# Performance work log

Measured on AMD Instinct MI355X. Metric: run time of the kernel, lower is better.

The kernel has to match this reference:

```python
import jax, jax.numpy as jnp
import numpy as np

B, S, D = 2, 2048, 768
H = 12
DK = D // H  # 64; dim_q = dim_k = dim_v
DFF = 3072
EPS = 1e-5


def layer_norm(x, w, b):
    mu = jnp.mean(x, axis=-1, keepdims=True)
    var = jnp.var(x, axis=-1, keepdims=True)
    return (x - mu) * jax.lax.rsqrt(var + EPS) * w + b


def setup_inputs() -> dict:
    key = jax.random.key(0)
    ks = jax.random.split(key, 12)
    s = 0.02
    return {
        "src": jax.random.normal(ks[0], (B, S, D), dtype=jnp.float32),
        # per-head projections stacked over heads: [H, D, DK]
        "Wq": jax.random.normal(ks[1], (H, D, DK), dtype=jnp.float32) * s,
        "bq": jnp.zeros((H, DK), dtype=jnp.float32),
        "Wk": jax.random.normal(ks[2], (H, D, DK), dtype=jnp.float32) * s,
        "bk": jnp.zeros((H, DK), dtype=jnp.float32),
        "Wv": jax.random.normal(ks[3], (H, D, DK), dtype=jnp.float32) * s,
        "bv": jnp.zeros((H, DK), dtype=jnp.float32),
        # output projection: [H*DK, D]
        "Wo": jax.random.normal(ks[4], (H * DK, D), dtype=jnp.float32) * s,
        "bo": jnp.zeros((D,), dtype=jnp.float32),
        "ln1_w": jnp.ones((D,), dtype=jnp.float32),
        "ln1_b": jnp.zeros((D,), dtype=jnp.float32),
        "W1": jax.random.normal(ks[5], (D, DFF), dtype=jnp.float32) * s,
        "b1": jnp.zeros((DFF,), dtype=jnp.float32),
        "W2": jax.random.normal(ks[6], (DFF, D), dtype=jnp.float32) * s,
        "b2": jnp.zeros((D,), dtype=jnp.float32),
        "ln2_w": jnp.ones((D,), dtype=jnp.float32),
        "ln2_b": jnp.zeros((D,), dtype=jnp.float32),
    }


def reference(src, Wq, bq, Wk, bk, Wv, bv, Wo, bo, ln1_w, ln1_b,
              W1, b1, W2, b2, ln2_w, ln2_b):
    # per-head q/k/v projections, batched over heads via einsum
    q = jnp.einsum('bsd,hdk->bhsk', src, Wq) + bq[None, :, None, :]
    k = jnp.einsum('bsd,hdk->bhsk', src, Wk) + bk[None, :, None, :]
    v = jnp.einsum('bsd,hdk->bhsk', src, Wv) + bv[None, :, None, :]
    scale = jnp.asarray(DK, src.dtype) ** 0.5
    scores = jnp.einsum('bhsk,bhtk->bhst', q, k) / scale  # [B,H,S,S]
    attn = jax.nn.softmax(scores, axis=-1)
    ctx = jnp.einsum('bhst,bhtk->bhsk', attn, v)
    # concat heads along feature dim (matches torch.cat over head outputs)
    ctx = ctx.transpose(0, 2, 1, 3).reshape(src.shape[0], src.shape[1], H * DK)
    attn_out = ctx @ Wo + bo
    x = layer_norm(src + attn_out, ln1_w, ln1_b)
    ff = jax.nn.relu(x @ W1 + b1) @ W2 + b2
    return layer_norm(x + ff, ln2_w, ln2_b)
```

## Files before the change

kernel.cpp:

```cpp
#include <hip/hip_runtime.h>
#include <hip/hip_bf16.h>

#define S_LEN 2048
#define DMODEL 768
#define NHEAD 12
#define DKH 64
#define DFF_K 3072
#define MROWS 4096
#define KSPLIT 2
#define KHALF (S_LEN / KSPLIT)

typedef __attribute__((ext_vector_type(8))) short bf16x8;
typedef __attribute__((ext_vector_type(8))) unsigned short us8;
typedef __attribute__((ext_vector_type(4))) float f32x4;

__device__ __forceinline__ float bfu2f(unsigned short u) {
  return __uint_as_float(((unsigned int)u) << 16);
}
__device__ __forceinline__ unsigned short f2bfu(float f) {
  __hip_bfloat16 h = __float2bfloat16(f);
  return *reinterpret_cast<unsigned short*>(&h);
}

__global__ __launch_bounds__(256) void convert_kernel(
    const float* __restrict__ in, unsigned short* __restrict__ out, int n4)
{
  const int i = blockIdx.x * 256 + threadIdx.x;
  if (i < n4) {
    float4 v = *(const float4*)(in + (size_t)i * 4);
    ushort4 o;
    o.x = f2bfu(v.x); o.y = f2bfu(v.y); o.z = f2bfu(v.z); o.w = f2bfu(v.w);
    *(ushort4*)(out + (size_t)i * 4) = o;
  }
}

__device__ __forceinline__ void transpose_conv_body(
    const float* in, unsigned short* out, int R, int Ctot, int head,
    int bx, int by, int tid)
{
  __shared__ float t[64][68];
  const int r0 = bx * 64;
  const int c0 = by * 64;
  const float* ib;
  int ld;
  if (head) { ib = in + (size_t)by * R * 64; ld = 64; }
  else      { ib = in + c0;                  ld = Ctot; }
  const int lr = tid >> 4;
  const int lc = (tid & 15) << 2;

#pragma unroll
  for (int rr = 0; rr < 4; ++rr) {
    const int row = rr * 16 + lr;
    float4 v = *(const float4*)(ib + (size_t)(r0 + row) * ld + lc);
    t[row][lc + 0] = v.x; t[row][lc + 1] = v.y;
    t[row][lc + 2] = v.z; t[row][lc + 3] = v.w;
  }
  __syncthreads();
#pragma unroll
  for (int rr = 0; rr < 4; ++rr) {
    const int oc = rr * 16 + lr;
    ushort4 o;
    o.x = f2bfu(t[lc + 0][oc]); o.y = f2bfu(t[lc + 1][oc]);
    o.z = f2bfu(t[lc + 2][oc]); o.w = f2bfu(t[lc + 3][oc]);
    *(ushort4*)(out + (size_t)(c0 + oc) * R + r0 + lc) = o;
  }
}

__global__ __launch_bounds__(256) void transpose_conv_kernel(
    const float* __restrict__ in, unsigned short* __restrict__ out,
    int R, int Ctot, int head)
{
  transpose_conv_body(in, out, R, Ctot, head, blockIdx.x, blockIdx.y, threadIdx.x);
}

__global__ __launch_bounds__(256) void transpose_conv4_kernel(
    const float* __restrict__ i0, const float* __restrict__ i1,
    const float* __restrict__ i2, const float* __restrict__ i3,
    unsigned short* __restrict__ o0, unsigned short* __restrict__ o1,
    unsigned short* __restrict__ o2, unsigned short* __restrict__ o3)
{
  const int z = blockIdx.z;
  const float* in = (z == 0) ? i0 : (z == 1) ? i1 : (z == 2) ? i2 : i3;
  unsigned short* out = (z == 0) ? o0 : (z == 1) ? o1 : (z == 2) ? o2 : o3;
  transpose_conv_body(in, out, DMODEL, DMODEL, (z < 3) ? 1 : 0,
                      blockIdx.x, blockIdx.y, threadIdx.x);
}

template<int BN>
__global__ __launch_bounds__(256) void mfma_gemm_kernel(
    const unsigned short* __restrict__ A,
    const unsigned short* __restrict__ BT,
    const float* __restrict__ bias,
    unsigned short* __restrict__ C,
    int K, int N, int relu, int klen, size_t out_stride)
{
  constexpr int WN = (BN == 128) ? 64 : 32;
  constexpr int NJ = WN / 16;
  __shared__ unsigned short As[128][40];
  __shared__ unsigned short Bs[BN][40];

  const int tid  = threadIdx.x;
  const int wid  = tid >> 6;
  const int lane = tid & 63;
  const int ml   = lane & 15;
  const int quad = lane >> 4;
  const int wm   = (wid & 1) * 64;
  const int wn   = (wid >> 1) * WN;
  const int row0 = blockIdx.x * 128;
  const int col0 = blockIdx.y * BN;
  const int zed  = blockIdx.z;
  const int kb0  = zed * klen;
  const int kend = kb0 + klen;

  const int sr = tid >> 2;
  const int sk = (tid & 3) << 3;

  const unsigned short* pA0 = A  + (size_t)(row0 + sr) * K + sk;
  const unsigned short* pA1 = A  + (size_t)(row0 + sr + 64) * K + sk;
  const unsigned short* pB0 = BT + (size_t)(col0 + sr) * K + sk;
  const unsigned short* pB1 = BT + (size_t)(col0 + sr + 64) * K + sk;

  f32x4 acc[4][NJ];
#pragma unroll
  for (int i = 0; i < 4; ++i)
#pragma unroll
    for (int j = 0; j < NJ; ++j)
#pragma unroll
      for (int r = 0; r < 4; ++r) acc[i][j][r] = 0.f;

  us8 ra0 = *(const us8*)(pA0 + kb0);
  us8 ra1 = *(const us8*)(pA1 + kb0);
  us8 rb0 = *(const us8*)(pB0 + kb0);
  us8 rb1;
  if (BN == 128) rb1 = *(const us8*)(pB1 + kb0);

  for (int k0 = kb0; k0 < kend; k0 += 32) {
    *(us8*)&As[sr][sk]      = ra0;
    *(us8*)&As[sr + 64][sk] = ra1;
    *(us8*)&Bs[sr][sk]      = rb0;
    if (BN == 128) *(us8*)&Bs[sr + 64][sk] = rb1;
    __syncthreads();

    const int kn = k0 + 32;
    if (kn < kend) {
      ra0 = *(const us8*)(pA0 + kn);
      ra1 = *(const us8*)(pA1 + kn);
      rb0 = *(const us8*)(pB0 + kn);
      if (BN == 128) rb1 = *(const us8*)(pB1 + kn);
    }

    bf16x8 af[4], bfr[NJ];
#pragma unroll
    for (int i = 0; i < 4; ++i)
      af[i] = *(const bf16x8*)&As[wm + i * 16 + ml][quad << 3];
#pragma unroll
    for (int j = 0; j < NJ; ++j)
      bfr[j] = *(const bf16x8*)&Bs[wn + j * 16 + ml][quad << 3];
#pragma unroll
    for (int i = 0; i < 4; ++i)
#pragma unroll
      for (int j = 0; j < NJ; ++j)
        acc[i][j] = __builtin_amdgcn_mfma_f32_16x16x32_bf16(
            af[i], bfr[j], acc[i][j], 0, 0, 0);
    __syncthreads();
  }

  unsigned short* Cz = C + (size_t)zed * out_stride;
#pragma unroll
  for (int j = 0; j < NJ; ++j) {
    const int col = col0 + wn + j * 16 + ml;
    const float bb = (zed == 0) ? bias[col] : 0.f;
#pragma unroll
    for (int i = 0; i < 4; ++i) {
      const int r0g = row0 + wm + i * 16 + (quad << 2);
#pragma unroll
      for (int r = 0; r < 4; ++r) {
        float v = acc[i][j][r] + bb;
        if (relu) v = fmaxf(v, 0.f);
        Cz[(size_t)(r0g + r) * N + col] = f2bfu(v);
      }
    }
  }
}

__global__ __launch_bounds__(256) void qkv_gemm_kernel(
    const unsigned short* __restrict__ A,
    const unsigned short* __restrict__ W0, const unsigned short* __restrict__ W1,
    const unsigned short* __restrict__ W2,
    const float* __restrict__ bq, const float* __restrict__ bk,
    const float* __restrict__ bv,
    unsigned short* __restrict__ C0, unsigned short* __restrict__ C1,
    unsigned short* __restrict__ C2)
{
  __shared__ unsigned short As[128][40];
  __shared__ unsigned short Bs[64][40];
  const int z = blockIdx.z;
  const unsigned short* BT = (z == 0) ? W0 : (z == 1) ? W1 : W2;
  const float* bias = (z == 0) ? bq : (z == 1) ? bk : bv;
  unsigned short* C = (z == 0) ? C0 : (z == 1) ? C1 : C2;
  const int K = DMODEL, N = DMODEL;

  const int tid  = threadIdx.x;
  const int wid  = tid >> 6;
  const int lane = tid & 63;
  const int ml   = lane & 15;
  const int quad = lane >> 4;
  const int wm   = (wid & 1) * 64;
  const int wn   = (wid >> 1) * 32;
  const int row0 = blockIdx.x * 128;
  const int col0 = blockIdx.y * 64;
  const int sr = tid >> 2;
  const int sk = (tid & 3) << 3;

  const unsigned short* pA0 = A  + (size_t)(row0 + sr) * K + sk;
  const unsigned short* pA1 = A  + (size_t)(row0 + sr + 64) * K + sk;
  const unsigned short* pB0 = BT + (size_t)(col0 + sr) * K + sk;

  f32x4 acc[4][2];
#pragma unroll
  for (int i = 0; i < 4; ++i)
#pragma unroll
    for (int j = 0; j < 2; ++j)
#pragma unroll
      for (int r = 0; r < 4; ++r) acc[i][j][r] = 0.f;

  us8 ra0 = *(const us8*)pA0;
  us8 ra1 = *(const us8*)pA1;
  us8 rb0 = *(const us8*)pB0;

  for (int k0 = 0; k0 < K; k0 += 32) {
    *(us8*)&As[sr][sk]      = ra0;
    *(us8*)&As[sr + 64][sk] = ra1;
    *(us8*)&Bs[sr][sk]      = rb0;
    __syncthreads();

    const int kn = k0 + 32;
    if (kn < K) {
      ra0 = *(const us8*)(pA0 + kn);
      ra1 = *(const us8*)(pA1 + kn);
      rb0 = *(const us8*)(pB0 + kn);
    }

    bf16x8 af[4], bfr[2];
#pragma unroll
    for (int i = 0; i < 4; ++i)
      af[i] = *(const bf16x8*)&As[wm + i * 16 + ml][quad << 3];
#pragma unroll
    for (int j = 0; j < 2; ++j)
      bfr[j] = *(const bf16x8*)&Bs[wn + j * 16 + ml][quad << 3];
#pragma unroll
    for (int i = 0; i < 4; ++i)
#pragma unroll
      for (int j = 0; j < 2; ++j)
        acc[i][j] = __builtin_amdgcn_mfma_f32_16x16x32_bf16(
            af[i], bfr[j], acc[i][j], 0, 0, 0);
    __syncthreads();
  }

#pragma unroll
  for (int j = 0; j < 2; ++j) {
    const int col = col0 + wn + j * 16 + ml;
    const float bb = bias[col];
#pragma unroll
    for (int i = 0; i < 4; ++i) {
      const int r0g = row0 + wm + i * 16 + (quad << 2);
      if (z == 2) {
        const int bb_ = r0g >> 11, s = r0g & 2047;
        const int hh = col >> 6, dd = col & 63;
        ushort4 o;
        o.x = f2bfu(acc[i][j][0] + bb); o.y = f2bfu(acc[i][j][1] + bb);
        o.z = f2bfu(acc[i][j][2] + bb); o.w = f2bfu(acc[i][j][3] + bb);
        *(ushort4*)(C + ((size_t)((bb_ * NHEAD + hh) * DKH + dd)) * S_LEN + s) = o;
      } else {
#pragma unroll
        for (int r = 0; r < 4; ++r)
          C[(size_t)(r0g + r) * N + col] = f2bfu(acc[i][j][r] + bb);
      }
    }
  }
}

#define FATS 72
#define SCL2E 0.1803368822f
__global__ __launch_bounds__(256) void flash_attn_mfma(
    const unsigned short* __restrict__ Q,
    const unsigned short* __restrict__ K,
    const unsigned short* __restrict__ VT,
    float* __restrict__ Opart,
    float* __restrict__ Lpart)
{
  __shared__ unsigned short Ks[64][FATS];
  __shared__ unsigned short Vs[64][FATS];
  __shared__ unsigned short QP[4][16][FATS];

  const int tid  = threadIdx.x;
  const int wid  = tid >> 6;
  const int lane = tid & 63;
  const int ml   = lane & 15;
  const int quad = lane >> 4;
  const int h    = blockIdx.x, b = blockIdx.y;
  const int q0   = (blockIdx.z >> 1) * 64;
  const int ks   = blockIdx.z & 1;
  const int kt0  = ks * KHALF;

  const size_t qkbase = ((size_t)b * S_LEN) * DMODEL + (size_t)h * DKH;
  const size_t vtbase = ((size_t)(b * NHEAD + h)) * DKH * S_LEN;

  const int sr = tid >> 2;
  const int sc = (tid & 3) << 4;

  {
    const unsigned short* qp = Q + qkbase + (size_t)(q0 + sr) * DMODEL + sc;
    *(us8*)&QP[sr >> 4][sr & 15][sc]     = *(const us8*)qp;
    *(us8*)&QP[sr >> 4][sr & 15][sc + 8] = *(const us8*)(qp + 8);
  }
  bf16x8 qf[2];
  qf[0] = *(const bf16x8*)&QP[wid][ml][quad << 3];
  qf[1] = *(const bf16x8*)&QP[wid][ml][32 + (quad << 3)];

  const unsigned short* pK = K + qkbase + (size_t)(kt0 + sr) * DMODEL + sc;
  const unsigned short* pV = VT + vtbase + (size_t)sr * S_LEN + kt0 + sc;

  float lsum = 0.f;
  f32x4 oacc[4];
#pragma unroll
  for (int dt = 0; dt < 4; ++dt)
#pragma unroll
    for (int r = 0; r < 4; ++r) oacc[dt][r] = 0.f;

  us8 rk0 = *(const us8*)(pK);
  us8 rk1 = *(const us8*)(pK + 8);
  us8 rv0 = *(const us8*)(pV);
  us8 rv1 = *(const us8*)(pV + 8);

  for (int kt = 0; kt < KHALF; kt += 64) {
    __syncthreads();
    *(us8*)&Ks[sr][sc]     = rk0;
    *(us8*)&Ks[sr][sc + 8] = rk1;
    *(us8*)&Vs[sr][sc]     = rv0;
    *(us8*)&Vs[sr][sc + 8] = rv1;
    __syncthreads();

    const int ktn = kt + 64;
    if (ktn < KHALF) {
      rk0 = *(const us8*)(pK + (size_t)ktn * DMODEL);
      rk1 = *(const us8*)(pK + (size_t)ktn * DMODEL + 8);
      rv0 = *(const us8*)(pV + ktn);
      rv1 = *(const us8*)(pV + ktn + 8);
    }

    f32x4 sacc[4];
#pragma unroll
    for (int mt = 0; mt < 4; ++mt)
#pragma unroll
      for (int r = 0; r < 4; ++r) sacc[mt][r] = 0.f;
#pragma unroll
    for (int mt = 0; mt < 4; ++mt) {
      bf16x8 kf0 = *(const bf16x8*)&Ks[mt * 16 + ml][quad << 3];
      bf16x8 kf1 = *(const bf16x8*)&Ks[mt * 16 + ml][32 + (quad << 3)];
      sacc[mt] = __builtin_amdgcn_mfma_f32_16x16x32_bf16(kf0, qf[0], sacc[mt], 0, 0, 0);
      sacc[mt] = __builtin_amdgcn_mfma_f32_16x16x32_bf16(kf1, qf[1], sacc[mt], 0, 0, 0);
    }

    float p[4][4];
#pragma unroll
    for (int mt2 = 0; mt2 < 4; ++mt2)
#pragma unroll
      for (int r = 0; r < 4; ++r) {
        const float e = exp2f(sacc[mt2][r] * SCL2E);
        p[mt2][r] = e;
        lsum += e;
      }

#pragma unroll
    for (int mt2 = 0; mt2 < 4; ++mt2) {
      ushort4 o;
      o.x = f2bfu(p[mt2][0]); o.y = f2bfu(p[mt2][1]);
      o.z = f2bfu(p[mt2][2]); o.w = f2bfu(p[mt2][3]);
      *(ushort4*)&QP[wid][ml][mt2 * 16 + (quad << 2)] = o;
    }
    bf16x8 pf0 = *(const bf16x8*)&QP[wid][ml][quad << 3];
    bf16x8 pf1 = *(const bf16x8*)&QP[wid][ml][32 + (quad << 3)];

#pragma unroll
    for (int dt = 0; dt < 4; ++dt) {
      bf16x8 vf0 = *(const bf16x8*)&Vs[dt * 16 + ml][quad << 3];
      bf16x8 vf1 = *(const bf16x8*)&Vs[dt * 16 + ml][32 + (quad << 3)];
      oacc[dt] = __builtin_amdgcn_mfma_f32_16x16x32_bf16(vf0, pf0, oacc[dt], 0, 0, 0);
      oacc[dt] = __builtin_amdgcn_mfma_f32_16x16x32_bf16(vf1, pf1, oacc[dt], 0, 0, 0);
    }
  }

  lsum += __shfl_xor(lsum, 16);
  lsum += __shfl_xor(lsum, 32);
  const int qrow = q0 + wid * 16 + ml;
  const size_t obase =
      ((((size_t)(ks * 2 + b)) * NHEAD + h) * S_LEN + qrow) * DKH;
#pragma unroll
  for (int dt = 0; dt < 4; ++dt)
    *(f32x4*)&Opart[obase + dt * 16 + (quad << 2)] = oacc[dt];
  if (quad == 0)
    Lpart[(((size_t)(ks * 2 + b)) * NHEAD + h) * S_LEN + qrow] = lsum;
}

__global__ __launch_bounds__(256) void attn_combine_kernel(
    const float* __restrict__ Op,
    const float* __restrict__ Lp,
    unsigned short* __restrict__ O)
{
  const int s = blockIdx.x & (S_LEN - 1);
  const int b = blockIdx.x >> 11;
  const int tid = threadIdx.x;
  const size_t ohalf = (size_t)2 * NHEAD * S_LEN * DKH;
  const size_t lhalf = (size_t)2 * NHEAD * S_LEN;
#pragma unroll
  for (int c = tid; c < DMODEL; c += 256) {
    const int hh = c >> 6, dd = c & 63;
    const size_t li = ((size_t)b * NHEAD + hh) * S_LEN + s;
    const size_t oi = li * DKH + dd;
    const float o = Op[oi] + Op[ohalf + oi];
    const float l = Lp[li] + Lp[lhalf + li];
    O[((size_t)b * S_LEN + s) * DMODEL + c] = f2bfu(o / l);
  }
}

__global__ __launch_bounds__(256) void add_ln_kernel(
    const void* __restrict__ X, const void* __restrict__ Y,
    const void* __restrict__ Y2,
    const float* __restrict__ w, const float* __restrict__ bvec,
    void* __restrict__ out, int xbf, int ybf, int obf)
{
  __shared__ float buf[DMODEL];
  __shared__ float rbuf[8];
  const int tid  = threadIdx.x;
  const int lane = tid & 63, wv = tid >> 6;
  const size_t base = (size_t)blockIdx.x * DMODEL;

  float s = 0.f, s2 = 0.f;
#pragma unroll
  for (int j = tid; j < DMODEL; j += 256) {
    float xv = xbf ? bfu2f(((const unsigned short*)X)[base + j])
                   : ((const float*)X)[base + j];
    float yv = ybf ? bfu2f(((const unsigned short*)Y)[base + j])
                   : ((const float*)Y)[base + j];
    float v = xv + yv;
    if (Y2) v += ybf ? bfu2f(((const unsigned short*)Y2)[base + j])
                     : ((const float*)Y2)[base + j];
    buf[j] = v; s += v; s2 += v * v;
  }
#pragma unroll
  for (int o = 32; o; o >>= 1) { s += __shfl_xor(s, o); s2 += __shfl_xor(s2, o); }
  if (lane == 0) { rbuf[wv] = s; rbuf[4 + wv] = s2; }
  __syncthreads();
  const float S  = rbuf[0] + rbuf[1] + rbuf[2] + rbuf[3];
  const float S2 = rbuf[4] + rbuf[5] + rbuf[6] + rbuf[7];
  const float mean = S * (1.f / (float)DMODEL);
  const float var  = S2 * (1.f / (float)DMODEL) - mean * mean;
  const float rstd = rsqrtf(var + 1e-5f);
#pragma unroll
  for (int j = tid; j < DMODEL; j += 256) {
    float v = (buf[j] - mean) * rstd * w[j] + bvec[j];
    if (obf) ((unsigned short*)out)[base + j] = f2bfu(v);
    else     ((float*)out)[base + j] = v;
  }
}

extern "C" void kernel_launch(void* const* d_in, const int* in_sizes, int n_in,
                              void* d_out, int out_size, void* d_ws, size_t ws_size,
                              hipStream_t stream) {
  const float* src  = (const float*)d_in[0];
  const float* Wq   = (const float*)d_in[1];
  const float* bq   = (const float*)d_in[2];
  const float* Wk   = (const float*)d_in[3];
  const float* bk   = (const float*)d_in[4];
  const float* Wv   = (const float*)d_in[5];
  const float* bv   = (const float*)d_in[6];
  const float* Wo   = (const float*)d_in[7];
  const float* bo   = (const float*)d_in[8];
  const float* ln1w = (const float*)d_in[9];
  const float* ln1b = (const float*)d_in[10];
  const float* W1   = (const float*)d_in[11];
  const float* b1   = (const float*)d_in[12];
  const float* W2   = (const float*)d_in[13];
  const float* b2   = (const float*)d_in[14];
  const float* ln2w = (const float*)d_in[15];
  const float* ln2b = (const float*)d_in[16];
  (void)ws_size; (void)in_sizes; (void)n_in; (void)out_size;

  unsigned short* p = (unsigned short*)d_ws;
  const size_t SEG = (size_t)MROWS * DMODEL;
  unsigned short* srcb = p; p += SEG;
  unsigned short* qb   = p; p += SEG;
  unsigned short* kb_  = p; p += SEG;
  unsigned short* vbT  = p; p += SEG;
  unsigned short* ctx  = p; p += SEG;
  unsigned short* ff   = p; p += (size_t)MROWS * DFF_K;
  unsigned short* wqt  = p; p += (size_t)DMODEL * DMODEL;
  unsigned short* wkt  = p; p += (size_t)DMODEL * DMODEL;
  unsigned short* wvt  = p; p += (size_t)DMODEL * DMODEL;
  unsigned short* wot  = p; p += (size_t)DMODEL * DMODEL;
  unsigned short* w1t  = p; p += (size_t)DMODEL * DFF_K;
  unsigned short* w2t  = p; p += (size_t)DMODEL * DFF_K;
  unsigned short* x1 = kb_;
  float* opart = (float*)ff;
  float* lpart = (float*)wqt;

  dim3 blk(256);

  convert_kernel<<<dim3(SEG / 1024), blk, 0, stream>>>(src, srcb, (int)(SEG / 4));
  transpose_conv4_kernel<<<dim3(12, 12, 4), blk, 0, stream>>>(
      Wq, Wk, Wv, Wo, wqt, wkt, wvt, wot);
  transpose_conv_kernel<<<dim3(12, 48), blk, 0, stream>>>(W1, w1t, DMODEL, DFF_K, 0);
  transpose_conv_kernel<<<dim3(48, 12), blk, 0, stream>>>(W2, w2t, DFF_K, DMODEL, 0);

  dim3 gqkv(MROWS / 128, DMODEL / 64, 3);
  qkv_gemm_kernel<<<gqkv, blk, 0, stream>>>(srcb, wqt, wkt, wvt, bq, bk, bv,
                                            qb, kb_, vbT);

  dim3 ga(NHEAD, 2, (S_LEN / 64) * KSPLIT);
  flash_attn_mfma<<<ga, blk, 0, stream>>>(qb, kb_, vbT, opart, lpart);
  attn_combine_kernel<<<dim3(MROWS), blk, 0, stream>>>(opart, lpart, ctx);

  dim3 gWo(MROWS / 128, DMODEL / 64, 2);
  mfma_gemm_kernel<64><<<gWo, blk, 0, stream>>>(ctx, wot, bo, qb,
                                                DMODEL, DMODEL, 0, DMODEL / 2, 2 * SEG);

  add_ln_kernel<<<dim3(MROWS), blk, 0, stream>>>(srcb, qb, vbT,
                                                 ln1w, ln1b, x1, 1, 1, 1);

  dim3 gF1(MROWS / 128, DFF_K / 128, 1);
  mfma_gemm_kernel<128><<<gF1, blk, 0, stream>>>(x1, w1t, b1, ff,
                                                 DMODEL, DFF_K, 1, DMODEL, 0);

  dim3 gW2(MROWS / 128, DMODEL / 64, 2);
  mfma_gemm_kernel<64><<<gW2, blk, 0, stream>>>(ff, w2t, b2, qb,
                                                DFF_K, DMODEL, 0, DFF_K / 2, 2 * SEG);

  add_ln_kernel<<<dim3(MROWS), blk, 0, stream>>>(x1, qb, vbT,
                                                 ln2w, ln2b, (float*)d_out, 1, 1, 0);
}
```

Before: 305.9 us.

## Double query rows per flash-attention block and XOR-swizzle shared-memory tiles

Each wave now handles 32 query rows (two 16-row MFMA tiles) instead of 16, so every K/V tile staged in shared memory feeds twice as many MFMAs and the grid shrinks by half. The padded LDS arrays are replaced with unpadded 64-wide rows using an XOR swizzle to avoid bank conflicts. Q fragments are loaded straight from global memory into registers instead of going through LDS. Register pressure roughly doubles for accumulators, which the launch-bounds hint of 3 blocks per CU is meant to keep in check. The smaller grid also lowers parallelism.

```diff
diff --git a/kernel.cpp b/kernel.cpp
--- a/kernel.cpp
+++ b/kernel.cpp
@@ -280,18 +280,17 @@
   }
 }
 
-#define FATS 72
 #define SCL2E 0.1803368822f
-__global__ __launch_bounds__(256) void flash_attn_mfma(
+__global__ __launch_bounds__(256, 3) void flash_attn_mfma(
     const unsigned short* __restrict__ Q,
     const unsigned short* __restrict__ K,
     const unsigned short* __restrict__ VT,
     float* __restrict__ Opart,
     float* __restrict__ Lpart)
 {
-  __shared__ unsigned short Ks[64][FATS];
-  __shared__ unsigned short Vs[64][FATS];
-  __shared__ unsigned short QP[4][16][FATS];
+  __shared__ unsigned short Ks[64][64];
+  __shared__ unsigned short Vs[64][64];
+  __shared__ unsigned short QP[4][2][16][64];
 
   const int tid  = threadIdx.x;
   const int wid  = tid >> 6;
@@ -299,46 +298,53 @@
   const int ml   = lane & 15;
   const int quad = lane >> 4;
   const int h    = blockIdx.x, b = blockIdx.y;
-  const int q0   = (blockIdx.z >> 1) * 64;
+  const int q0   = (blockIdx.z >> 1) * 128;
   const int ks   = blockIdx.z & 1;
   const int kt0  = ks * KHALF;
 
   const size_t qkbase = ((size_t)b * S_LEN) * DMODEL + (size_t)h * DKH;
   const size_t vtbase = ((size_t)(b * NHEAD + h)) * DKH * S_LEN;
 
-  const int sr = tid >> 2;
-  const int sc = (tid & 3) << 4;
-
-  {
-    const unsigned short* qp = Q + qkbase + (size_t)(q0 + sr) * DMODEL + sc;
-    *(us8*)&QP[sr >> 4][sr & 15][sc]     = *(const us8*)qp;
-    *(us8*)&QP[sr >> 4][sr & 15][sc + 8] = *(const us8*)(qp + 8);
-  }
-  bf16x8 qf[2];
-  qf[0] = *(const bf16x8*)&QP[wid][ml][quad << 3];
-  qf[1] = *(const bf16x8*)&QP[wid][ml][32 + (quad << 3)];
-
-  const unsigned short* pK = K + qkbase + (size_t)(kt0 + sr) * DMODEL + sc;
-  const unsigned short* pV = VT + vtbase + (size_t)sr * S_LEN + kt0 + sc;
-
-  float lsum = 0.f;
-  f32x4 oacc[4];
+  const int sr  = tid >> 2;
+  const int scb = (tid & 3) << 5;
+  const int ssw = (sr & 7) << 4;
+  const int fsw = (ml & 7) << 4;
+
+  char* ksrow = (char*)&Ks[sr][0];
+  char* vsrow = (char*)&Vs[sr][0];
+
+  const int qrA = q0 + wid * 32 + ml;
+  const int qrB = qrA + 16;
+  const unsigned short* qpg = Q + qkbase;
+  bf16x8 qfA0 = *(const bf16x8*)(qpg + (size_t)qrA * DMODEL + (quad << 3));
+  bf16x8 qfA1 = *(const bf16x8*)(qpg + (size_t)qrA * DMODEL + 32 + (quad << 3));
+  bf16x8 qfB0 = *(const bf16x8*)(qpg + (size_t)qrB * DMODEL + (quad << 3));
+  bf16x8 qfB1 = *(const bf16x8*)(qpg + (size_t)qrB * DMODEL + 32 + (quad << 3));
+
+  const unsigned short* pK = K + qkbase + (size_t)(kt0 + sr) * DMODEL + (scb >> 1);
+  const unsigned short* pV = VT + vtbase + (size_t)sr * S_LEN + kt0 + (scb >> 1);
+
+  float lsumA = 0.f, lsumB = 0.f;
+  f32x4 oaccA[4], oaccB[4];
 #pragma unroll
   for (int dt = 0; dt < 4; ++dt)
 #pragma unroll
-    for (int r = 0; r < 4; ++r) oacc[dt][r] = 0.f;
+    for (int r = 0; r < 4; ++r) { oaccA[dt][r] = 0.f; oaccB[dt][r] = 0.f; }
 
   us8 rk0 = *(const us8*)(pK);
   us8 rk1 = *(const us8*)(pK + 8);
   us8 rv0 = *(const us8*)(pV);
   us8 rv1 = *(const us8*)(pV + 8);
 
+  char* qpA = (char*)&QP[wid][0][ml][0];
+  char* qpB = (char*)&QP[wid][1][ml][0];
+
   for (int kt = 0; kt < KHALF; kt += 64) {
     __syncthreads();
-    *(us8*)&Ks[sr][sc]     = rk0;
-    *(us8*)&Ks[sr][sc + 8] = rk1;
-    *(us8*)&Vs[sr][sc]     = rv0;
-    *(us8*)&Vs[sr][sc + 8] = rv1;
+    *(us8*)(ksrow + ((scb +  0) ^ ssw)) = rk0;
+    *(us8*)(ksrow + ((scb + 16) ^ ssw)) = rk1;
+    *(us8*)(vsrow + ((scb +  0) ^ ssw)) = rv0;
+    *(us8*)(vsrow + ((scb + 16) ^ ssw)) = rv1;
     __syncthreads();
 
     const int ktn = kt + 64;
@@ -349,58 +355,70 @@
       rv1 = *(const us8*)(pV + ktn + 8);
     }
 
-    f32x4 sacc[4];
+    f32x4 sA[4], sB[4];
 #pragma unroll
     for (int mt = 0; mt < 4; ++mt)
 #pragma unroll
-      for (int r = 0; r < 4; ++r) sacc[mt][r] = 0.f;
+      for (int r = 0; r < 4; ++r) { sA[mt][r] = 0.f; sB[mt][r] = 0.f; }
 #pragma unroll
     for (int mt = 0; mt < 4; ++mt) {
-      bf16x8 kf0 = *(const bf16x8*)&Ks[mt * 16 + ml][quad << 3];
-      bf16x8 kf1 = *(const bf16x8*)&Ks[mt * 16 + ml][32 + (quad << 3)];
-      sacc[mt] = __builtin_amdgcn_mfma_f32_16x16x32_bf16(kf0, qf[0], sacc[mt], 0, 0, 0);
-      sacc[mt] = __builtin_amdgcn_mfma_f32_16x16x32_bf16(kf1, qf[1], sacc[mt], 0, 0, 0);
-    }
-
-    float p[4][4];
-#pragma unroll
-    for (int mt2 = 0; mt2 < 4; ++mt2)
-#pragma unroll
-      for (int r = 0; r < 4; ++r) {
-        const float e = exp2f(sacc[mt2][r] * SCL2E);
-        p[mt2][r] = e;
-        lsum += e;
-      }
-
-#pragma unroll
-    for (int mt2 = 0; mt2 < 4; ++mt2) {
-      ushort4 o;
-      o.x = f2bfu(p[mt2][0]); o.y = f2bfu(p[mt2][1]);
-      o.z = f2bfu(p[mt2][2]); o.w = f2bfu(p[mt2][3]);
-      *(ushort4*)&QP[wid][ml][mt2 * 16 + (quad << 2)] = o;
-    }
-    bf16x8 pf0 = *(const bf16x8*)&QP[wid][ml][quad << 3];
-    bf16x8 pf1 = *(const bf16x8*)&QP[wid][ml][32 + (quad << 3)];
+      char* kr = (char*)&Ks[mt * 16 + ml][0];
+      bf16x8 kf0 = *(const bf16x8*)(kr + (((quad << 4) +  0) ^ fsw));
+      bf16x8 kf1 = *(const bf16x8*)(kr + (((quad << 4) + 64) ^ fsw));
+      sA[mt] = __builtin_amdgcn_mfma_f32_16x16x32_bf16(kf0, qfA0, sA[mt], 0, 0, 0);
+      sA[mt] = __builtin_amdgcn_mfma_f32_16x16x32_bf16(kf1, qfA1, sA[mt], 0, 0, 0);
+      sB[mt] = __builtin_amdgcn_mfma_f32_16x16x32_bf16(kf0, qfB0, sB[mt], 0, 0, 0);
+      sB[mt] = __builtin_amdgcn_mfma_f32_16x16x32_bf16(kf1, qfB1, sB[mt], 0, 0, 0);
+    }
+
+#pragma unroll
+    for (int mt = 0; mt < 4; ++mt) {
+      float e0 = exp2f(sA[mt][0] * SCL2E), e1 = exp2f(sA[mt][1] * SCL2E),
+            e2 = exp2f(sA[mt][2] * SCL2E), e3 = exp2f(sA[mt][3] * SCL2E);
+      lsumA += (e0 + e1) + (e2 + e3);
+      ushort4 oA;
+      oA.x = f2bfu(e0); oA.y = f2bfu(e1); oA.z = f2bfu(e2); oA.w = f2bfu(e3);
+      *(ushort4*)(qpA + (((mt << 5) + (quad << 3)) ^ fsw)) = oA;
+      e0 = exp2f(sB[mt][0] * SCL2E); e1 = exp2f(sB[mt][1] * SCL2E);
+      e2 = exp2f(sB[mt][2] * SCL2E); e3 = exp2f(sB[mt][3] * SCL2E);
+      lsumB += (e0 + e1) + (e2 + e3);
+      ushort4 oB;
+      oB.x = f2bfu(e0); oB.y = f2bfu(e1); oB.z = f2bfu(e2); oB.w = f2bfu(e3);
+      *(ushort4*)(qpB + (((mt << 5) + (quad << 3)) ^ fsw)) = oB;
+    }
+    bf16x8 pfA0 = *(const bf16x8*)(qpA + (((quad << 4) +  0) ^ fsw));
+    bf16x8 pfA1 = *(const bf16x8*)(qpA + (((quad << 4) + 64) ^ fsw));
+    bf16x8 pfB0 = *(const bf16x8*)(qpB + (((quad << 4) +  0) ^ fsw));
+    bf16x8 pfB1 = *(const bf16x8*)(qpB + (((quad << 4) + 64) ^ fsw));
 
 #pragma unroll
     for (int dt = 0; dt < 4; ++dt) {
-      bf16x8 vf0 = *(const bf16x8*)&Vs[dt * 16 + ml][quad << 3];
-      bf16x8 vf1 = *(const bf16x8*)&Vs[dt * 16 + ml][32 + (quad << 3)];
-      oacc[dt] = __builtin_amdgcn_mfma_f32_16x16x32_bf16(vf0, pf0, oacc[dt], 0, 0, 0);
-      oacc[dt] = __builtin_amdgcn_mfma_f32_16x16x32_bf16(vf1, pf1, oacc[dt], 0, 0, 0);
-    }
-  }
-
-  lsum += __shfl_xor(lsum, 16);
-  lsum += __shfl_xor(lsum, 32);
-  const int qrow = q0 + wid * 16 + ml;
-  const size_t obase =
-      ((((size_t)(ks * 2 + b)) * NHEAD + h) * S_LEN + qrow) * DKH;
-#pragma unroll
-  for (int dt = 0; dt < 4; ++dt)
-    *(f32x4*)&Opart[obase + dt * 16 + (quad << 2)] = oacc[dt];
-  if (quad == 0)
-    Lpart[(((size_t)(ks * 2 + b)) * NHEAD + h) * S_LEN + qrow] = lsum;
+      char* vr = (char*)&Vs[dt * 16 + ml][0];
+      bf16x8 vf0 = *(const bf16x8*)(vr + (((quad << 4) +  0) ^ fsw));
+      bf16x8 vf1 = *(const bf16x8*)(vr + (((quad << 4) + 64) ^ fsw));
+      oaccA[dt] = __builtin_amdgcn_mfma_f32_16x16x32_bf16(vf0, pfA0, oaccA[dt], 0, 0, 0);
+      oaccA[dt] = __builtin_amdgcn_mfma_f32_16x16x32_bf16(vf1, pfA1, oaccA[dt], 0, 0, 0);
+      oaccB[dt] = __builtin_amdgcn_mfma_f32_16x16x32_bf16(vf0, pfB0, oaccB[dt], 0, 0, 0);
+      oaccB[dt] = __builtin_amdgcn_mfma_f32_16x16x32_bf16(vf1, pfB1, oaccB[dt], 0, 0, 0);
+    }
+  }
+
+  lsumA += __shfl_xor(lsumA, 16);
+  lsumA += __shfl_xor(lsumA, 32);
+  lsumB += __shfl_xor(lsumB, 16);
+  lsumB += __shfl_xor(lsumB, 32);
+  const size_t lbase = (((size_t)(ks * 2 + b)) * NHEAD + h) * S_LEN;
+  const size_t obaseA = (lbase + qrA) * DKH;
+  const size_t obaseB = (lbase + qrB) * DKH;
+#pragma unroll
+  for (int dt = 0; dt < 4; ++dt) {
+    *(f32x4*)&Opart[obaseA + dt * 16 + (quad << 2)] = oaccA[dt];
+    *(f32x4*)&Opart[obaseB + dt * 16 + (quad << 2)] = oaccB[dt];
+  }
+  if (quad == 0) {
+    Lpart[lbase + qrA] = lsumA;
+    Lpart[lbase + qrB] = lsumB;
+  }
 }
 
 __global__ __launch_bounds__(256) void attn_combine_kernel(
@@ -517,7 +535,7 @@
   qkv_gemm_kernel<<<gqkv, blk, 0, stream>>>(srcb, wqt, wkt, wvt, bq, bk, bv,
                                             qb, kb_, vbT);
 
-  dim3 ga(NHEAD, 2, (S_LEN / 64) * KSPLIT);
+  dim3 ga(NHEAD, 2, (S_LEN / 128) * KSPLIT);
   flash_attn_mfma<<<ga, blk, 0, stream>>>(qb, kb_, vbT, opart, lpart);
   attn_combine_kernel<<<dim3(MROWS), blk, 0, stream>>>(opart, lpart, ctx);
 
```

Result: faster. 299.3 us (-2.1%).
